# Kernel optimization log

Measured on AMD Instinct MI355X. Metric: run time of the kernel, lower is better.

The kernel has to match this reference:

```python
import jax, jax.numpy as jnp
import numpy as np

N_NODES = 50000
N_EDGES = 800000
N_GRAPHS = 128
F_IN = 256
H = 256
DH = 64
NC = 2


def _lin_init(k, fin, fout):
    s = 1.0 / np.sqrt(fin)
    return jax.random.uniform(k, (fin, fout), jnp.float32, -s, s)


def setup_inputs() -> dict:
    key = jax.random.key(0)
    ks = jax.random.split(key, 12)
    x = jax.random.normal(ks[0], (N_NODES, F_IN), jnp.float32)
    edge_index = jax.random.randint(ks[1], (2, N_EDGES), 0, N_NODES, jnp.int32)
    edge_attr = jax.random.uniform(ks[2], (N_EDGES,), jnp.float32)
    batch = jnp.sort(jax.random.randint(ks[3], (N_NODES,), 0, N_GRAPHS, jnp.int32))
    return {
        "x": x, "edge_index": edge_index, "edge_attr": edge_attr, "batch": batch,
        "W1": _lin_init(ks[4], F_IN, H), "b1": jnp.zeros((H,), jnp.float32),
        "W2": _lin_init(ks[5], H, H), "b2": jnp.zeros((H,), jnp.float32),
        "W3": _lin_init(ks[6], H, H), "b3": jnp.zeros((H,), jnp.float32),
        "L1w": _lin_init(ks[7], H, DH), "L1b": jnp.zeros((DH,), jnp.float32),
        "L2w": _lin_init(ks[8], DH, DH // 2), "L2b": jnp.zeros((DH // 2,), jnp.float32),
        "L3w": _lin_init(ks[9], DH // 2, NC), "L3b": jnp.zeros((NC,), jnp.float32),
    }


def reference(x, edge_index, edge_attr, batch, W1, b1, W2, b2, W3, b3,
              L1w, L1b, L2w, L2b, L3w, L3b):
    src, dst = edge_index[0], edge_index[1]
    # GCN normalization with self loops (weight 1): deg includes self-loop
    deg = jax.ops.segment_sum(edge_attr, dst, num_segments=N_NODES) + 1.0
    dinv = jnp.where(deg > 0, jax.lax.rsqrt(deg), 0.0)
    norm = dinv[src] * edge_attr * dinv[dst]          # [E]
    self_coef = dinv * dinv                            # [N], self-loop norm

    def gcn(h, W, b):
        h = h @ W                                      # [N, H]
        agg = jax.ops.segment_sum(norm[:, None] * h[src], dst, num_segments=N_NODES)
        return agg + self_coef[:, None] * h + b

    c1 = gcn(x, W1, b1)
    h = jax.nn.relu(c1)                                # dropout is eval-mode no-op
    c2 = gcn(h, W2, b2)
    h = jax.nn.relu(c2)
    c3 = gcn(h, W3, b3)
    h = jax.nn.relu(c3)

    # global mean pool over graphs
    sums = jax.ops.segment_sum(h, batch, num_segments=N_GRAPHS)
    cnt = jax.ops.segment_sum(jnp.ones((N_NODES,), h.dtype), batch, num_segments=N_GRAPHS)
    pooled = sums / jnp.clip(cnt, 1.0)[:, None]        # [B, H]

    o = jax.nn.relu(pooled @ L1w + L1b)
    o = jax.nn.relu(o @ L2w + L2b)
    out = jax.nn.relu(o @ L3w + L3b)                   # [B, NC]
    return (out, pooled, c1, c2, c3)
```

## Files before the change

kernel.cpp:

```cpp
#include <hip/hip_runtime.h>

#define N_NODES  50000
#define N_EDGES  800000
#define N_GRAPHS 128
#define FDIM     256

typedef __attribute__((ext_vector_type(8))) short short8;
typedef __attribute__((ext_vector_type(4))) float f32x4;

__device__ __forceinline__ unsigned short f2bf(float f) {
    union { float f; unsigned int u; } v; v.f = f;
    unsigned int x = v.u;
    unsigned int r = (x + 0x7FFFu + ((x >> 16) & 1u)) >> 16;
    return (unsigned short)r;
}

__device__ __forceinline__ float bf2f(unsigned short u) {
    union { unsigned int i; float f; } v;
    v.i = ((unsigned int)u) << 16;
    return v.f;
}


__global__ void k_zero(float* deg, int* cnt, int n) {
    int i = blockIdx.x * blockDim.x + threadIdx.x;
    if (i < n) { deg[i] = 0.0f; cnt[i] = 0; }
}

__global__ void k_deg(const int* __restrict__ dst, const float* __restrict__ ea,
                      float* deg, int* cnt, int E) {
    int e = blockIdx.x * blockDim.x + threadIdx.x;
    if (e < E) {
        int d = dst[e];
        atomicAdd(&deg[d], ea[e]);
        atomicAdd(&cnt[d], 1);
    }
}


__global__ __launch_bounds__(1024) void k_scan1(const int* __restrict__ cnt,
                                                const float* __restrict__ deg,
                                                float* __restrict__ dinv,
                                                int* row_ptr, int* partial, int n) {
    __shared__ int buf[2][1024];
    int tid = threadIdx.x;
    int i = blockIdx.x * 1024 + tid;
    if (i < n) dinv[i] = rsqrtf(deg[i] + 1.0f);
    int v = (i < n) ? cnt[i] : 0;
    buf[0][tid] = v;
    __syncthreads();
    int pb = 0;
    for (int off = 1; off < 1024; off <<= 1) {
        int t = buf[pb][tid];
        if (tid >= off) t += buf[pb][tid - off];
        buf[1 - pb][tid] = t;
        pb = 1 - pb;
        __syncthreads();
    }
    int incl = buf[pb][tid];
    if (i < n) row_ptr[i] = incl - v;
    if (tid == 1023) partial[blockIdx.x] = incl;
}

__global__ void k_scan2(int* partial, int nb, int* totalp) {
    int l = threadIdx.x;
    int v = (l < nb) ? partial[l] : 0;
    int orig = v;
    for (int off = 1; off < 64; off <<= 1) {
        int t = __shfl_up(v, off);
        if (l >= off) v += t;
    }
    if (l < nb) partial[l] = v - orig;
    if (l == nb - 1) *totalp = v;
}

__global__ void k_scan3(int* row_ptr, int* cursor, const int* __restrict__ partial, int n) {
    int i = blockIdx.x * blockDim.x + threadIdx.x;
    if (i < n) {
        int v = row_ptr[i] + partial[i >> 10];
        row_ptr[i] = v;
        cursor[i] = v;
    }
}


__global__ void k_scatter(const int* __restrict__ src, const int* __restrict__ dst,
                          const float* __restrict__ ea,
                          const float* __restrict__ dinv,
                          int* cursor, int2* cv, int E) {
    int e = blockIdx.x * blockDim.x + threadIdx.x;
    if (e < E) {
        int d = dst[e];
        int s = src[e];
        int p = atomicAdd(&cursor[d], 1);
        cv[p] = make_int2(s << 9, __float_as_int(ea[e] * dinv[s]));
    }
}

__global__ void k_repack3(const float* __restrict__ W1, const float* __restrict__ W2,
                          const float* __restrict__ W3, unsigned short* __restrict__ Wp) {
    int tid = blockIdx.x * blockDim.x + threadIdx.x;
    int w = tid >> 16;
    int t = tid & 65535;
    const float* W = (w == 0) ? W1 : ((w == 1) ? W2 : W3);
    int j = t & 7;
    int l = (t >> 3) & 63;
    int c = (t >> 9) & 15;
    int s = t >> 13;
    int k = s * 32 + ((l >> 4) * 8) + j;
    int n = c * 16 + (l & 15);
    Wp[tid] = f2bf(W[k * 256 + n]);
}

__global__ void k_xcast(const float* __restrict__ x, unsigned short* __restrict__ Xb, int n4) {
    int i = blockIdx.x * blockDim.x + threadIdx.x;
    if (i < n4) {
        float4 v = ((const float4*)x)[i];
        ((ushort4*)Xb)[i] = make_ushort4(f2bf(v.x), f2bf(v.y), f2bf(v.z), f2bf(v.w));
    }
}

__global__ __launch_bounds__(256) void k_agg_cs(const unsigned short* __restrict__ Hb,
                                                const int* __restrict__ rowptr,
                                                const int2* __restrict__ cv,
                                                const float* __restrict__ dinv,
                                                unsigned short* __restrict__ S,
                                                int M, int rowBlocks) {
    int pass = blockIdx.x / rowBlocks;
    int rb   = blockIdx.x - pass * rowBlocks;
    int wave = threadIdx.x >> 6;
    int lane = threadIdx.x & 63;
    int sub  = lane >> 4;
    int l16  = lane & 15;
    int n = rb * 4 + wave;
    if (n >= M) return;
    unsigned int cb2 = (unsigned int)((pass * 64 + l16 * 4) * 2);
    const char* Hc = (const char*)Hb;

    float a0 = 0.f, a1 = 0.f, a2 = 0.f, a3 = 0.f;
    int e0 = rowptr[n], e1 = rowptr[n + 1];

    int e = e0 + sub;
    for (; e + 12 < e1; e += 16) {
        int2 p0 = cv[e];
        int2 p1 = cv[e + 4];
        int2 p2 = cv[e + 8];
        int2 p3 = cv[e + 12];
        ushort4 h0 = *(const ushort4*)(Hc + ((unsigned int)p0.x + cb2));
        ushort4 h1 = *(const ushort4*)(Hc + ((unsigned int)p1.x + cb2));
        ushort4 h2 = *(const ushort4*)(Hc + ((unsigned int)p2.x + cb2));
        ushort4 h3 = *(const ushort4*)(Hc + ((unsigned int)p3.x + cb2));
        float v0 = __int_as_float(p0.y);
        float v1 = __int_as_float(p1.y);
        float v2 = __int_as_float(p2.y);
        float v3 = __int_as_float(p3.y);
        a0 = fmaf(v0, bf2f(h0.x), a0); a1 = fmaf(v0, bf2f(h0.y), a1);
        a2 = fmaf(v0, bf2f(h0.z), a2); a3 = fmaf(v0, bf2f(h0.w), a3);
        a0 = fmaf(v1, bf2f(h1.x), a0); a1 = fmaf(v1, bf2f(h1.y), a1);
        a2 = fmaf(v1, bf2f(h1.z), a2); a3 = fmaf(v1, bf2f(h1.w), a3);
        a0 = fmaf(v2, bf2f(h2.x), a0); a1 = fmaf(v2, bf2f(h2.y), a1);
        a2 = fmaf(v2, bf2f(h2.z), a2); a3 = fmaf(v2, bf2f(h2.w), a3);
        a0 = fmaf(v3, bf2f(h3.x), a0); a1 = fmaf(v3, bf2f(h3.y), a1);
        a2 = fmaf(v3, bf2f(h3.z), a2); a3 = fmaf(v3, bf2f(h3.w), a3);
    }
    for (; e < e1; e += 4) {
        int2 p = cv[e];
        ushort4 h = *(const ushort4*)(Hc + ((unsigned int)p.x + cb2));
        float v = __int_as_float(p.y);
        a0 = fmaf(v, bf2f(h.x), a0); a1 = fmaf(v, bf2f(h.y), a1);
        a2 = fmaf(v, bf2f(h.z), a2); a3 = fmaf(v, bf2f(h.w), a3);
    }
    a0 += __shfl_xor(a0, 16); a0 += __shfl_xor(a0, 32);
    a1 += __shfl_xor(a1, 16); a1 += __shfl_xor(a1, 32);
    a2 += __shfl_xor(a2, 16); a2 += __shfl_xor(a2, 32);
    a3 += __shfl_xor(a3, 16); a3 += __shfl_xor(a3, 32);

    if (sub == 0) {
        float di = dinv[n];
        float sc = di * di;
        unsigned int rowb = ((unsigned int)n << 9) + cb2;
        ushort4 hn = *(const ushort4*)(Hc + rowb);
        *(ushort4*)((char*)S + rowb) =
            make_ushort4(f2bf(fmaf(di, a0, sc * bf2f(hn.x))),
                         f2bf(fmaf(di, a1, sc * bf2f(hn.y))),
                         f2bf(fmaf(di, a2, sc * bf2f(hn.z))),
                         f2bf(fmaf(di, a3, sc * bf2f(hn.w))));
    }
}

template<bool RELU>
__global__ __launch_bounds__(256) void k_agg(const float* __restrict__ H,
                                             const int* __restrict__ rowptr,
                                             const int2* __restrict__ cv,
                                             const float* __restrict__ dinv,
                                             unsigned short* __restrict__ S, int M) {
    int wave = threadIdx.x >> 6;
    int lane = threadIdx.x & 63;
    int n = blockIdx.x * 4 + wave;
    if (n >= M) return;
    int f4 = lane * 4;

    float a0 = 0.f, a1 = 0.f, a2 = 0.f, a3 = 0.f;
    int e0 = rowptr[n], e1 = rowptr[n + 1];
    for (int e = e0; e < e1; e++) {
        int2 p = cv[e];
        int s = p.x >> 9;
        float v = __int_as_float(p.y);
        float4 h = *(const float4*)(H + (size_t)s * 256 + f4);
        if (RELU) {
            h.x = fmaxf(h.x, 0.f); h.y = fmaxf(h.y, 0.f);
            h.z = fmaxf(h.z, 0.f); h.w = fmaxf(h.w, 0.f);
        }
        a0 = fmaf(v, h.x, a0); a1 = fmaf(v, h.y, a1);
        a2 = fmaf(v, h.z, a2); a3 = fmaf(v, h.w, a3);
    }
    float di = dinv[n];
    float sc = di * di;
    float4 hn = *(const float4*)(H + (size_t)n * 256 + f4);
    if (RELU) {
        hn.x = fmaxf(hn.x, 0.f); hn.y = fmaxf(hn.y, 0.f);
        hn.z = fmaxf(hn.z, 0.f); hn.w = fmaxf(hn.w, 0.f);
    }
    *(ushort4*)(S + (size_t)n * 256 + f4) =
        make_ushort4(f2bf(fmaf(di, a0, sc * hn.x)), f2bf(fmaf(di, a1, sc * hn.y)),
                     f2bf(fmaf(di, a2, sc * hn.z)), f2bf(fmaf(di, a3, sc * hn.w)));
}

template<bool NT>
__global__ __launch_bounds__(256, 2) void k_gemm2(const unsigned short* __restrict__ S,
                                                  const unsigned short* __restrict__ Wp,
                                                  const float* __restrict__ bias,
                                                  float* __restrict__ C,
                                                  unsigned short* __restrict__ Hb,
                                                  int nTiles) {
    int wave = threadIdx.x >> 6;
    int lane = threadIdx.x & 63;
    int q    = lane >> 4;
    int m16  = lane & 15;
    const short8* wp8 = (const short8*)Wp;

    short8 b[8][4];
#pragma unroll
    for (int s = 0; s < 8; s++)
#pragma unroll
        for (int cc = 0; cc < 4; cc++)
            b[s][cc] = wp8[(s * 16 + wave * 4 + cc) * 64 + lane];

    float bv[4];
#pragma unroll
    for (int cc = 0; cc < 4; cc++) bv[cc] = bias[(wave * 4 + cc) * 16 + m16];

#pragma unroll 1
    for (int rt = blockIdx.x; rt < nTiles; rt += gridDim.x) {
        int arow = rt * 16 + m16;
        short8 a[8];
#pragma unroll
        for (int s = 0; s < 8; s++)
            a[s] = *(const short8*)(S + (size_t)arow * 256 + s * 32 + q * 8);

        f32x4 acc[4];
#pragma unroll
        for (int cc = 0; cc < 4; cc++) acc[cc] = (f32x4){0.f, 0.f, 0.f, 0.f};

#pragma unroll
        for (int s = 0; s < 8; s++)
#pragma unroll
            for (int cc = 0; cc < 4; cc++)
                acc[cc] = __builtin_amdgcn_mfma_f32_16x16x32_bf16(a[s], b[s][cc], acc[cc], 0, 0, 0);

        int orow0 = rt * 16 + q * 4;
#pragma unroll
        for (int cc = 0; cc < 4; cc++) {
            int colv = (wave * 4 + cc) * 16 + m16;
#pragma unroll
            for (int r = 0; r < 4; r++) {
                float ov = acc[cc][r] + bv[cc];
                if (NT) __builtin_nontemporal_store(ov, &C[(size_t)(orow0 + r) * 256 + colv]);
                else    C[(size_t)(orow0 + r) * 256 + colv] = ov;
            }
        }
        if (Hb != nullptr) {
#pragma unroll
            for (int cc = 0; cc < 4; cc++) {
                int colv = (wave * 4 + cc) * 16 + m16;
#pragma unroll
                for (int r = 0; r < 4; r++)
                    Hb[(size_t)(orow0 + r) * 256 + colv] = f2bf(fmaxf(acc[cc][r] + bv[cc], 0.f));
            }
        }
    }
}

__global__ __launch_bounds__(1024) void k_pool(const float* __restrict__ C3,
                                               const int* __restrict__ batch, int N,
                                               float* __restrict__ pooled) {
    int g = blockIdx.x;
    __shared__ int range[2];
    __shared__ float part[4][256];
    if (threadIdx.x == 0 && threadIdx.y == 0) {
        int lo = 0, hi = N;
        while (lo < hi) { int mid = (lo + hi) >> 1; if (batch[mid] < g) lo = mid + 1; else hi = mid; }
        range[0] = lo;
        int lo2 = lo, hi2 = N;
        while (lo2 < hi2) { int mid = (lo2 + hi2) >> 1; if (batch[mid] < g + 1) lo2 = mid + 1; else hi2 = mid; }
        range[1] = lo2;
    }
    __syncthreads();
    int start = range[0], end = range[1];
    int f = threadIdx.x;
    float s = 0.f;
    for (int i = start + threadIdx.y; i < end; i += 4)
        s += fmaxf(C3[(size_t)i * 256 + f], 0.f);
    part[threadIdx.y][f] = s;
    __syncthreads();
    if (threadIdx.y == 0) {
        float tot = part[0][f] + part[1][f] + part[2][f] + part[3][f];
        int cnt = end - start;
        pooled[g * 256 + f] = tot / (float)(cnt > 0 ? cnt : 1);
    }
}

__global__ __launch_bounds__(64) void k_mlp(const float* __restrict__ pooled,
                                            const float* __restrict__ L1w,
                                            const float* __restrict__ L1b,
                                            const float* __restrict__ L2w,
                                            const float* __restrict__ L2b,
                                            const float* __restrict__ L3w,
                                            const float* __restrict__ L3b,
                                            float* __restrict__ out) {
    int g = blockIdx.x;
    int j = threadIdx.x;
    __shared__ float o1[64];
    __shared__ float o2[32];
    float s = L1b[j];
    const float* p = pooled + g * 256;
    for (int k = 0; k < 256; k++) s = fmaf(p[k], L1w[k * 64 + j], s);
    o1[j] = fmaxf(s, 0.f);
    __syncthreads();
    if (j < 32) {
        float s2 = L2b[j];
        for (int k = 0; k < 64; k++) s2 = fmaf(o1[k], L2w[k * 32 + j], s2);
        o2[j] = fmaxf(s2, 0.f);
    }
    __syncthreads();
    if (j < 2) {
        float s3 = L3b[j];
        for (int k = 0; k < 32; k++) s3 = fmaf(o2[k], L3w[k * 2 + j], s3);
        out[g * 2 + j] = fmaxf(s3, 0.f);
    }
}

extern "C" void kernel_launch(void* const* d_in, const int* in_sizes, int n_in,
                              void* d_out, int out_size, void* d_ws, size_t ws_size,
                              hipStream_t stream) {
    const float* x   = (const float*)d_in[0];
    const int*   ei  = (const int*)d_in[1];
    const float* ea  = (const float*)d_in[2];
    const int*   bat = (const int*)d_in[3];
    const float* W1  = (const float*)d_in[4];
    const float* b1  = (const float*)d_in[5];
    const float* W2  = (const float*)d_in[6];
    const float* b2  = (const float*)d_in[7];
    const float* W3  = (const float*)d_in[8];
    const float* b3  = (const float*)d_in[9];
    const float* L1w = (const float*)d_in[10];
    const float* L1b = (const float*)d_in[11];
    const float* L2w = (const float*)d_in[12];
    const float* L2b = (const float*)d_in[13];
    const float* L3w = (const float*)d_in[14];
    const float* L3b = (const float*)d_in[15];

    const int N = N_NODES, E = N_EDGES;
    const int* srcp = ei;
    const int* dstp = ei + E;

    float* out_p    = (float*)d_out;
    float* pooled_p = out_p + 256;
    float* c1_p     = out_p + 33024;
    float* c2_p     = c1_p + (size_t)N * FDIM;
    float* c3_p     = c2_p + (size_t)N * FDIM;

    char* ws = (char*)d_ws;
    size_t off = 0;
    unsigned short* Sb  = (unsigned short*)(ws + off); off += (size_t)(N + 64) * FDIM * 2;
    unsigned short* Wp1 = (unsigned short*)(ws + off); off += 65536 * 2;
    unsigned short* Wp2 = (unsigned short*)(ws + off); off += 65536 * 2;
    unsigned short* Wp3 = (unsigned short*)(ws + off); off += 65536 * 2;
    float* dinv    = (float*)(ws + off); off += (size_t)N * 4;
    float* deg     = (float*)(ws + off); off += (size_t)N * 4;
    int*   cnt     = (int*)(ws + off);   off += (size_t)N * 4;
    int*   row_ptr = (int*)(ws + off);   off += ((size_t)N + 16) * 4;
    int*   cursor  = (int*)(ws + off);   off += (size_t)N * 4;
    int2*  cv      = (int2*)(ws + off);  off += (size_t)E * 8;
    int*   partial = (int*)(ws + off);   off += 64 * 4;
    unsigned short* Hb = (unsigned short*)(ws + off); off += (size_t)(N + 64) * FDIM * 2;
    bool use_bf = (ws_size >= off);
    (void)n_in; (void)in_sizes; (void)out_size;

    int nb256 = (N + 255) / 256;
    int eb256 = (E + 255) / 256;
    int nb1024 = (N + 1023) / 1024;

    k_zero<<<nb256, 256, 0, stream>>>(deg, cnt, N);
    k_deg<<<eb256, 256, 0, stream>>>(dstp, ea, deg, cnt, E);
    k_scan1<<<nb1024, 1024, 0, stream>>>(cnt, deg, dinv, row_ptr, partial, N);
    k_scan2<<<1, 64, 0, stream>>>(partial, nb1024, row_ptr + N);
    k_scan3<<<nb256, 256, 0, stream>>>(row_ptr, cursor, partial, N);
    k_scatter<<<eb256, 256, 0, stream>>>(srcp, dstp, ea, dinv, cursor, cv, E);
    k_repack3<<<768, 256, 0, stream>>>(W1, W2, W3, Wp1);

    int rowBlocks   = (N + 3) / 4;
    int agg_grid    = rowBlocks * 4;
    int nTiles      = (N + 15) / 16;
    int gemm_blocks = 512;

    if (use_bf) {
        k_xcast<<<(N * 64 + 255) / 256, 256, 0, stream>>>(x, Hb, N * 64);
        k_agg_cs<<<agg_grid, 256, 0, stream>>>(Hb, row_ptr, cv, dinv, Sb, N, rowBlocks);
        k_gemm2<true><<<gemm_blocks, 256, 0, stream>>>(Sb, Wp1, b1, c1_p, Hb, nTiles);
        k_agg_cs<<<agg_grid, 256, 0, stream>>>(Hb, row_ptr, cv, dinv, Sb, N, rowBlocks);
        k_gemm2<true><<<gemm_blocks, 256, 0, stream>>>(Sb, Wp2, b2, c2_p, Hb, nTiles);
        k_agg_cs<<<agg_grid, 256, 0, stream>>>(Hb, row_ptr, cv, dinv, Sb, N, rowBlocks);
        k_gemm2<false><<<gemm_blocks, 256, 0, stream>>>(Sb, Wp3, b3, c3_p, nullptr, nTiles);
    } else {
        int agg_blocks = (N + 3) / 4;
        k_agg<false><<<agg_blocks, 256, 0, stream>>>(x, row_ptr, cv, dinv, Sb, N);
        k_gemm2<false><<<gemm_blocks, 256, 0, stream>>>(Sb, Wp1, b1, c1_p, nullptr, nTiles);
        k_agg<true><<<agg_blocks, 256, 0, stream>>>(c1_p, row_ptr, cv, dinv, Sb, N);
        k_gemm2<false><<<gemm_blocks, 256, 0, stream>>>(Sb, Wp2, b2, c2_p, nullptr, nTiles);
        k_agg<true><<<agg_blocks, 256, 0, stream>>>(c2_p, row_ptr, cv, dinv, Sb, N);
        k_gemm2<false><<<gemm_blocks, 256, 0, stream>>>(Sb, Wp3, b3, c3_p, nullptr, nTiles);
    }

    dim3 pb(256, 4);
    k_pool<<<N_GRAPHS, pb, 0, stream>>>(c3_p, bat, N, pooled_p);
    k_mlp<<<N_GRAPHS, 64, 0, stream>>>(pooled_p, L1w, L1b, L2w, L2b, L3w, L3b, out_p);
}
```

Baseline: 741.3 us.

## Fuse sparse aggregation with MFMA GEMM through LDS tiles and ping-pong bf16 buffers

Merges the per-layer aggregation kernel and the GEMM kernel into one persistent kernel. Each 16-row tile is aggregated by waves into shared memory and then multiplied with register-resident weights. This removes the bf16 S round-trip through global memory and half the launches. The cost is that the aggregation now runs one row per wave with the full 256 features per lane group, instead of splitting rows across 4 feature passes, which changes gather parallelism and occupancy. Two Hb buffers ping-pong so the output of one layer does not overwrite the input another block may still read.

```diff
diff --git a/kernel.cpp b/kernel.cpp
--- a/kernel.cpp
+++ b/kernel.cpp
@@ -120,71 +120,118 @@
     }
 }
 
-__global__ __launch_bounds__(256) void k_agg_cs(const unsigned short* __restrict__ Hb,
-                                                const int* __restrict__ rowptr,
-                                                const int2* __restrict__ cv,
-                                                const float* __restrict__ dinv,
-                                                unsigned short* __restrict__ S,
-                                                int M, int rowBlocks) {
-    int pass = blockIdx.x / rowBlocks;
-    int rb   = blockIdx.x - pass * rowBlocks;
+template<bool NT, bool EMIT_HB>
+__global__ __launch_bounds__(256, 2) void k_fused(const unsigned short* __restrict__ HbIn,
+                                                  const int* __restrict__ rowptr,
+                                                  const int2* __restrict__ cv,
+                                                  const float* __restrict__ dinv,
+                                                  const unsigned short* __restrict__ Wp,
+                                                  const float* __restrict__ bias,
+                                                  float* __restrict__ C,
+                                                  unsigned short* __restrict__ HbOut,
+                                                  int nTiles) {
+    __shared__ unsigned short S_lds[16][264];
     int wave = threadIdx.x >> 6;
     int lane = threadIdx.x & 63;
-    int sub  = lane >> 4;
-    int l16  = lane & 15;
-    int n = rb * 4 + wave;
-    if (n >= M) return;
-    unsigned int cb2 = (unsigned int)((pass * 64 + l16 * 4) * 2);
-    const char* Hc = (const char*)Hb;
-
-    float a0 = 0.f, a1 = 0.f, a2 = 0.f, a3 = 0.f;
-    int e0 = rowptr[n], e1 = rowptr[n + 1];
-
-    int e = e0 + sub;
-    for (; e + 12 < e1; e += 16) {
-        int2 p0 = cv[e];
-        int2 p1 = cv[e + 4];
-        int2 p2 = cv[e + 8];
-        int2 p3 = cv[e + 12];
-        ushort4 h0 = *(const ushort4*)(Hc + ((unsigned int)p0.x + cb2));
-        ushort4 h1 = *(const ushort4*)(Hc + ((unsigned int)p1.x + cb2));
-        ushort4 h2 = *(const ushort4*)(Hc + ((unsigned int)p2.x + cb2));
-        ushort4 h3 = *(const ushort4*)(Hc + ((unsigned int)p3.x + cb2));
-        float v0 = __int_as_float(p0.y);
-        float v1 = __int_as_float(p1.y);
-        float v2 = __int_as_float(p2.y);
-        float v3 = __int_as_float(p3.y);
-        a0 = fmaf(v0, bf2f(h0.x), a0); a1 = fmaf(v0, bf2f(h0.y), a1);
-        a2 = fmaf(v0, bf2f(h0.z), a2); a3 = fmaf(v0, bf2f(h0.w), a3);
-        a0 = fmaf(v1, bf2f(h1.x), a0); a1 = fmaf(v1, bf2f(h1.y), a1);
-        a2 = fmaf(v1, bf2f(h1.z), a2); a3 = fmaf(v1, bf2f(h1.w), a3);
-        a0 = fmaf(v2, bf2f(h2.x), a0); a1 = fmaf(v2, bf2f(h2.y), a1);
-        a2 = fmaf(v2, bf2f(h2.z), a2); a3 = fmaf(v2, bf2f(h2.w), a3);
-        a0 = fmaf(v3, bf2f(h3.x), a0); a1 = fmaf(v3, bf2f(h3.y), a1);
-        a2 = fmaf(v3, bf2f(h3.z), a2); a3 = fmaf(v3, bf2f(h3.w), a3);
-    }
-    for (; e < e1; e += 4) {
-        int2 p = cv[e];
-        ushort4 h = *(const ushort4*)(Hc + ((unsigned int)p.x + cb2));
-        float v = __int_as_float(p.y);
-        a0 = fmaf(v, bf2f(h.x), a0); a1 = fmaf(v, bf2f(h.y), a1);
-        a2 = fmaf(v, bf2f(h.z), a2); a3 = fmaf(v, bf2f(h.w), a3);
-    }
-    a0 += __shfl_xor(a0, 16); a0 += __shfl_xor(a0, 32);
-    a1 += __shfl_xor(a1, 16); a1 += __shfl_xor(a1, 32);
-    a2 += __shfl_xor(a2, 16); a2 += __shfl_xor(a2, 32);
-    a3 += __shfl_xor(a3, 16); a3 += __shfl_xor(a3, 32);
-
-    if (sub == 0) {
-        float di = dinv[n];
-        float sc = di * di;
-        unsigned int rowb = ((unsigned int)n << 9) + cb2;
-        ushort4 hn = *(const ushort4*)(Hc + rowb);
-        *(ushort4*)((char*)S + rowb) =
-            make_ushort4(f2bf(fmaf(di, a0, sc * bf2f(hn.x))),
-                         f2bf(fmaf(di, a1, sc * bf2f(hn.y))),
-                         f2bf(fmaf(di, a2, sc * bf2f(hn.z))),
-                         f2bf(fmaf(di, a3, sc * bf2f(hn.w))));
+    int q    = lane >> 4;
+    int m16  = lane & 15;
+    const short8* wp8 = (const short8*)Wp;
+    const char* Hc = (const char*)HbIn;
+
+    short8 b[8][4];
+#pragma unroll
+    for (int s = 0; s < 8; s++)
+#pragma unroll
+        for (int cc = 0; cc < 4; cc++)
+            b[s][cc] = wp8[(s * 16 + wave * 4 + cc) * 64 + lane];
+
+    float bv[4];
+#pragma unroll
+    for (int cc = 0; cc < 4; cc++) bv[cc] = bias[(wave * 4 + cc) * 16 + m16];
+
+    unsigned int cb2 = (unsigned int)(lane * 8);
+
+#pragma unroll 1
+    for (int rt = blockIdx.x; rt < nTiles; rt += gridDim.x) {
+#pragma unroll 1
+        for (int rr = 0; rr < 4; rr++) {
+            int n = rt * 16 + wave * 4 + rr;
+            float a0 = 0.f, a1 = 0.f, a2 = 0.f, a3 = 0.f;
+            int e0 = rowptr[n], e1 = rowptr[n + 1];
+            int e = e0;
+#pragma unroll 1
+            for (; e + 4 <= e1; e += 4) {
+                int2 p0 = cv[e], p1 = cv[e + 1], p2 = cv[e + 2], p3 = cv[e + 3];
+                ushort4 h0 = *(const ushort4*)(Hc + ((unsigned int)p0.x + cb2));
+                ushort4 h1 = *(const ushort4*)(Hc + ((unsigned int)p1.x + cb2));
+                ushort4 h2 = *(const ushort4*)(Hc + ((unsigned int)p2.x + cb2));
+                ushort4 h3 = *(const ushort4*)(Hc + ((unsigned int)p3.x + cb2));
+                float v0 = __int_as_float(p0.y), v1 = __int_as_float(p1.y);
+                float v2 = __int_as_float(p2.y), v3 = __int_as_float(p3.y);
+                a0 = fmaf(v0, bf2f(h0.x), a0); a1 = fmaf(v0, bf2f(h0.y), a1);
+                a2 = fmaf(v0, bf2f(h0.z), a2); a3 = fmaf(v0, bf2f(h0.w), a3);
+                a0 = fmaf(v1, bf2f(h1.x), a0); a1 = fmaf(v1, bf2f(h1.y), a1);
+                a2 = fmaf(v1, bf2f(h1.z), a2); a3 = fmaf(v1, bf2f(h1.w), a3);
+                a0 = fmaf(v2, bf2f(h2.x), a0); a1 = fmaf(v2, bf2f(h2.y), a1);
+                a2 = fmaf(v2, bf2f(h2.z), a2); a3 = fmaf(v2, bf2f(h2.w), a3);
+                a0 = fmaf(v3, bf2f(h3.x), a0); a1 = fmaf(v3, bf2f(h3.y), a1);
+                a2 = fmaf(v3, bf2f(h3.z), a2); a3 = fmaf(v3, bf2f(h3.w), a3);
+            }
+#pragma unroll 1
+            for (; e < e1; e++) {
+                int2 p = cv[e];
+                ushort4 h = *(const ushort4*)(Hc + ((unsigned int)p.x + cb2));
+                float v = __int_as_float(p.y);
+                a0 = fmaf(v, bf2f(h.x), a0); a1 = fmaf(v, bf2f(h.y), a1);
+                a2 = fmaf(v, bf2f(h.z), a2); a3 = fmaf(v, bf2f(h.w), a3);
+            }
+            float di = dinv[n];
+            float sc = di * di;
+            ushort4 hn = *(const ushort4*)(Hc + (((unsigned int)n << 9) + cb2));
+            *(ushort4*)(&S_lds[wave * 4 + rr][lane * 4]) =
+                make_ushort4(f2bf(fmaf(di, a0, sc * bf2f(hn.x))),
+                             f2bf(fmaf(di, a1, sc * bf2f(hn.y))),
+                             f2bf(fmaf(di, a2, sc * bf2f(hn.z))),
+                             f2bf(fmaf(di, a3, sc * bf2f(hn.w))));
+        }
+        __syncthreads();
+
+        short8 a[8];
+#pragma unroll
+        for (int s = 0; s < 8; s++)
+            a[s] = *(const short8*)(&S_lds[m16][s * 32 + q * 8]);
+
+        f32x4 acc[4];
+#pragma unroll
+        for (int cc = 0; cc < 4; cc++) acc[cc] = (f32x4){0.f, 0.f, 0.f, 0.f};
+
+#pragma unroll
+        for (int s = 0; s < 8; s++)
+#pragma unroll
+            for (int cc = 0; cc < 4; cc++)
+                acc[cc] = __builtin_amdgcn_mfma_f32_16x16x32_bf16(a[s], b[s][cc], acc[cc], 0, 0, 0);
+
+        int orow0 = rt * 16 + q * 4;
+#pragma unroll
+        for (int cc = 0; cc < 4; cc++) {
+            int colv = (wave * 4 + cc) * 16 + m16;
+#pragma unroll
+            for (int r = 0; r < 4; r++) {
+                float ov = acc[cc][r] + bv[cc];
+                if (NT) __builtin_nontemporal_store(ov, &C[(size_t)(orow0 + r) * 256 + colv]);
+                else    C[(size_t)(orow0 + r) * 256 + colv] = ov;
+            }
+        }
+        if (EMIT_HB) {
+#pragma unroll
+            for (int cc = 0; cc < 4; cc++) {
+                int colv = (wave * 4 + cc) * 16 + m16;
+#pragma unroll
+                for (int r = 0; r < 4; r++)
+                    HbOut[(size_t)(orow0 + r) * 256 + colv] = f2bf(fmaxf(acc[cc][r] + bv[cc], 0.f));
+            }
+        }
+        __syncthreads();
     }
 }
 
@@ -226,12 +273,10 @@
                      f2bf(fmaf(di, a2, sc * hn.z)), f2bf(fmaf(di, a3, sc * hn.w)));
 }
 
-template<bool NT>
 __global__ __launch_bounds__(256, 2) void k_gemm2(const unsigned short* __restrict__ S,
                                                   const unsigned short* __restrict__ Wp,
                                                   const float* __restrict__ bias,
                                                   float* __restrict__ C,
-                                                  unsigned short* __restrict__ Hb,
                                                   int nTiles) {
     int wave = threadIdx.x >> 6;
     int lane = threadIdx.x & 63;
@@ -273,20 +318,8 @@
         for (int cc = 0; cc < 4; cc++) {
             int colv = (wave * 4 + cc) * 16 + m16;
 #pragma unroll
-            for (int r = 0; r < 4; r++) {
-                float ov = acc[cc][r] + bv[cc];
-                if (NT) __builtin_nontemporal_store(ov, &C[(size_t)(orow0 + r) * 256 + colv]);
-                else    C[(size_t)(orow0 + r) * 256 + colv] = ov;
-            }
-        }
-        if (Hb != nullptr) {
-#pragma unroll
-            for (int cc = 0; cc < 4; cc++) {
-                int colv = (wave * 4 + cc) * 16 + m16;
-#pragma unroll
-                for (int r = 0; r < 4; r++)
-                    Hb[(size_t)(orow0 + r) * 256 + colv] = f2bf(fmaxf(acc[cc][r] + bv[cc], 0.f));
-            }
+            for (int r = 0; r < 4; r++)
+                C[(size_t)(orow0 + r) * 256 + colv] = acc[cc][r] + bv[cc];
         }
     }
 }
@@ -393,7 +426,8 @@
     int*   cursor  = (int*)(ws + off);   off += (size_t)N * 4;
     int2*  cv      = (int2*)(ws + off);  off += (size_t)E * 8;
     int*   partial = (int*)(ws + off);   off += 64 * 4;
-    unsigned short* Hb = (unsigned short*)(ws + off); off += (size_t)(N + 64) * FDIM * 2;
+    unsigned short* HbA = (unsigned short*)(ws + off); off += (size_t)(N + 64) * FDIM * 2;
+    unsigned short* HbB = (unsigned short*)(ws + off); off += (size_t)(N + 64) * FDIM * 2;
     bool use_bf = (ws_size >= off);
     (void)n_in; (void)in_sizes; (void)out_size;
 
@@ -409,27 +443,22 @@
     k_scatter<<<eb256, 256, 0, stream>>>(srcp, dstp, ea, dinv, cursor, cv, E);
     k_repack3<<<768, 256, 0, stream>>>(W1, W2, W3, Wp1);
 
-    int rowBlocks   = (N + 3) / 4;
-    int agg_grid    = rowBlocks * 4;
-    int nTiles      = (N + 15) / 16;
-    int gemm_blocks = 512;
+    int nTiles       = N / 16;
+    int fused_blocks = 512;
 
     if (use_bf) {
-        k_xcast<<<(N * 64 + 255) / 256, 256, 0, stream>>>(x, Hb, N * 64);
-        k_agg_cs<<<agg_grid, 256, 0, stream>>>(Hb, row_ptr, cv, dinv, Sb, N, rowBlocks);
-        k_gemm2<true><<<gemm_blocks, 256, 0, stream>>>(Sb, Wp1, b1, c1_p, Hb, nTiles);
-        k_agg_cs<<<agg_grid, 256, 0, stream>>>(Hb, row_ptr, cv, dinv, Sb, N, rowBlocks);
-        k_gemm2<true><<<gemm_blocks, 256, 0, stream>>>(Sb, Wp2, b2, c2_p, Hb, nTiles);
-        k_agg_cs<<<agg_grid, 256, 0, stream>>>(Hb, row_ptr, cv, dinv, Sb, N, rowBlocks);
-        k_gemm2<false><<<gemm_blocks, 256, 0, stream>>>(Sb, Wp3, b3, c3_p, nullptr, nTiles);
+        k_xcast<<<(N * 64 + 255) / 256, 256, 0, stream>>>(x, HbA, N * 64);
+        k_fused<true,  true ><<<fused_blocks, 256, 0, stream>>>(HbA, row_ptr, cv, dinv, Wp1, b1, c1_p, HbB, nTiles);
+        k_fused<true,  true ><<<fused_blocks, 256, 0, stream>>>(HbB, row_ptr, cv, dinv, Wp2, b2, c2_p, HbA, nTiles);
+        k_fused<false, false><<<fused_blocks, 256, 0, stream>>>(HbA, row_ptr, cv, dinv, Wp3, b3, c3_p, HbB, nTiles);
     } else {
         int agg_blocks = (N + 3) / 4;
         k_agg<false><<<agg_blocks, 256, 0, stream>>>(x, row_ptr, cv, dinv, Sb, N);
-        k_gemm2<false><<<gemm_blocks, 256, 0, stream>>>(Sb, Wp1, b1, c1_p, nullptr, nTiles);
+        k_gemm2<<<fused_blocks, 256, 0, stream>>>(Sb, Wp1, b1, c1_p, nTiles);
         k_agg<true><<<agg_blocks, 256, 0, stream>>>(c1_p, row_ptr, cv, dinv, Sb, N);
-        k_gemm2<false><<<gemm_blocks, 256, 0, stream>>>(Sb, Wp2, b2, c2_p, nullptr, nTiles);
+        k_gemm2<<<fused_blocks, 256, 0, stream>>>(Sb, Wp2, b2, c2_p, nTiles);
         k_agg<true><<<agg_blocks, 256, 0, stream>>>(c2_p, row_ptr, cv, dinv, Sb, N);
-        k_gemm2<false><<<gemm_blocks, 256, 0, stream>>>(Sb, Wp3, b3, c3_p, nullptr, nTiles);
+        k_gemm2<<<fused_blocks, 256, 0, stream>>>(Sb, Wp3, b3, c3_p, nTiles);
     }
 
     dim3 pb(256, 4);
```

Measured after the change: 786.2 us. 6.1% more time.
